# Performance work log

Hardware: AMD Instinct MI355X
Metric: run time of the kernel (lower is better)

The kernel has to match this reference:

```python
import jax, jax.numpy as jnp
import numpy as np

DIM = 1536
HEADS = 12
HD = DIM // HEADS  # 128
EPS = 1e-6
SINK_SIZE = 1          # frames
MAX_ATTN = 1920        # tokens (sliding window)


def setup_inputs() -> dict:
    key = jax.random.key(0)
    ks = jax.random.split(key, 10)
    B = 1
    F, H, W = 8, 16, 24
    L = F * H * W  # 3072
    s = 0.02
    inp = {
        "x": jax.random.normal(ks[0], (B, L, DIM), jnp.float32),
        "seq_lens": jnp.array([L], jnp.int32),
        "grid_sizes": jnp.array([[F, H, W]], jnp.int32),
        "freqs": jax.random.normal(ks[1], (1024, HD // 2, 2), jnp.float32),
        "wq": jax.random.normal(ks[2], (DIM, DIM), jnp.float32) * s,
        "bq": jnp.zeros((DIM,), jnp.float32),
        "wk": jax.random.normal(ks[3], (DIM, DIM), jnp.float32) * s,
        "bk": jnp.zeros((DIM,), jnp.float32),
        "wv": jax.random.normal(ks[4], (DIM, DIM), jnp.float32) * s,
        "bv": jnp.zeros((DIM,), jnp.float32),
        "wo": jax.random.normal(ks[5], (DIM, DIM), jnp.float32) * s,
        "bo": jnp.zeros((DIM,), jnp.float32),
        "nq_w": jnp.ones((DIM,), jnp.float32),
        "nk_w": jnp.ones((DIM,), jnp.float32),
    }
    return inp


def _rmsnorm(x, w):
    # WanRMSNorm: x * rsqrt(mean(x^2) + eps) * weight
    return x * jax.lax.rsqrt(jnp.mean(x * x, axis=-1, keepdims=True) + EPS) * w


def _rope(x, F, H, W, fc):
    # x: [B, L, n, d]; fc: complex [1024, d//2]
    B, L, n, d = x.shape
    c = d // 2
    c1 = c - 2 * (c // 3)  # temporal split
    c2 = c // 3
    f0, f1, f2 = fc[:, :c1], fc[:, c1:c1 + c2], fc[:, c1 + c2:]
    fr = jnp.concatenate([
        jnp.broadcast_to(f0[:F, None, None, :], (F, H, W, c1)),
        jnp.broadcast_to(f1[None, :H, None, :], (F, H, W, c2)),
        jnp.broadcast_to(f2[None, None, :W, :], (F, H, W, c2)),
    ], axis=-1).reshape(L, 1, c)  # [L, 1, c]
    xp = x.reshape(B, L, n, c, 2)
    xc = jax.lax.complex(xp[..., 0], xp[..., 1])  # [B, L, n, c]
    xr = xc * fr[None]
    return jnp.stack([jnp.real(xr), jnp.imag(xr)], axis=-1).reshape(B, L, n, d)


def reference(x, seq_lens, grid_sizes, freqs, wq, bq, wk, bk, wv, bv, wo, bo, nq_w, nk_w):
    B, L, _ = x.shape
    gs = np.asarray(grid_sizes)[0]
    F, H, W = int(gs[0]), int(gs[1]), int(gs[2])
    fs = H * W  # frame_seqlen
    sink = SINK_SIZE * fs

    q = _rmsnorm(x @ wq.T + bq, nq_w).reshape(B, L, HEADS, HD)
    k = _rmsnorm(x @ wk.T + bk, nk_w).reshape(B, L, HEADS, HD)
    v = (x @ wv.T + bv).reshape(B, L, HEADS, HD)

    fc = jax.lax.complex(freqs[..., 0], freqs[..., 1])  # [1024, HD//2]
    q = _rope(q, F, H, W, fc)
    k = _rope(k, F, H, W, fc)

    # sink + windowed frame-causal block mask (flex_attention block_mask)
    idx = jnp.arange(L)
    qf = idx // fs
    kf = idx // fs
    mask = (kf[None, :] <= qf[:, None]) & (
        (idx[None, :] < sink) | (idx[None, :] >= (qf[:, None] + 1) * fs - MAX_ATTN)
    )  # [L, L]

    scale = 1.0 / np.float32(np.sqrt(HD))
    scores = jnp.einsum('bqnd,bknd->bnqk', q, k) * scale
    scores = jnp.where(mask[None, None], scores, jnp.float32(-1e30))
    attn = jax.nn.softmax(scores, axis=-1)
    out = jnp.einsum('bnqk,bknd->bqnd', attn, v).reshape(B, L, DIM)
    return out @ wo.T + bo
```

## Files before the change

kernel.cpp:

```cpp
#include <hip/hip_runtime.h>
#include <stdint.h>

#define DIMC 1536
#define LTOK 3072
#define HEADS 12
#define HD 128
#define FS 384
#define MAXATTN 1920
#define HTOK 1152
#define NHT 1920

typedef __attribute__((ext_vector_type(4))) float f32x4;
typedef __attribute__((ext_vector_type(8))) short bf16x8;
typedef __attribute__((ext_vector_type(4))) unsigned int u32x4;

__device__ __forceinline__ unsigned short f2bf(float f) {
  union { float f; unsigned int u; } c; c.f = f;
  unsigned int u = c.u + 0x7fffu + ((c.u >> 16) & 1u);
  return (unsigned short)(u >> 16);
}
__device__ __forceinline__ float bf2f(unsigned short s) {
  union { unsigned int u; float f; } c; c.u = (unsigned int)s << 16; return c.f;
}

__device__ __forceinline__ void dma16(const void* g, void* l) {
  __builtin_amdgcn_global_load_lds(
      (const __attribute__((address_space(1))) unsigned int*)g,
      (__attribute__((address_space(3))) unsigned int*)l, 16, 0, 0);
}

__global__ __launch_bounds__(256)
void cvt_all_k(const float* __restrict__ x, const float* __restrict__ wq,
               const float* __restrict__ wk, const float* __restrict__ wv,
               const float* __restrict__ wo,
               unsigned short* __restrict__ xb, unsigned short* __restrict__ wqb,
               unsigned short* __restrict__ wkb, unsigned short* __restrict__ wvb,
               unsigned short* __restrict__ wob)
{
  const int i = blockIdx.x * 256 + threadIdx.x;
  const int n0 = LTOK * DIMC / 4;
  const int nw = DIMC * DIMC / 4;
  const float* src; unsigned short* dst; int off;
  if (i < n0) { src = x; dst = xb; off = i; }
  else {
    int j = i - n0; int w = j / nw; off = j - w * nw;
    src = (w == 0) ? wq : (w == 1) ? wk : (w == 2) ? wv : wo;
    dst = (w == 0) ? wqb : (w == 1) ? wkb : (w == 2) ? wvb : wob;
  }
  float4 f = ((const float4*)src)[off];
  uint2 o;
  o.x = (unsigned int)f2bf(f.x) | ((unsigned int)f2bf(f.y) << 16);
  o.y = (unsigned int)f2bf(f.z) | ((unsigned int)f2bf(f.w) << 16);
  ((uint2*)dst)[off] = o;
}

__global__ __launch_bounds__(256)
void gemm_qkv(const unsigned short* __restrict__ A,
              const unsigned short* __restrict__ B0,
              const unsigned short* __restrict__ B1,
              const unsigned short* __restrict__ B2,
              const float* __restrict__ bias0,
              const float* __restrict__ bias1,
              const float* __restrict__ bias2,
              unsigned short* __restrict__ o0, unsigned short* __restrict__ o1,
              unsigned short* __restrict__ o2)
{
  const int z = blockIdx.z;
  const unsigned short* Bw = (z == 0) ? B0 : (z == 1) ? B1 : B2;
  const float* bias = (z == 0) ? bias0 : (z == 1) ? bias1 : bias2;
  unsigned short* outp = (z == 0) ? o0 : (z == 1) ? o1 : o2;

  __shared__ __align__(16) unsigned short lA[128 * 32];
  __shared__ __align__(16) unsigned short lB[128 * 32];

  const int tid = threadIdx.x;
  const int wave = tid >> 6;
  const int lane = tid & 63;
  const int m0 = blockIdx.y * 128;
  const int n0 = blockIdx.x * 128;
  const int wm = (wave >> 1) * 64;
  const int wn = (wave & 1) * 64;

  f32x4 acc[4][4] = {};

  const int srow = tid >> 2;
  const int scol = (tid & 3) * 8;
  const int fr = lane & 15;
  const int fk = (lane >> 4) * 8;

  unsigned short* la0 = &lA[srow * 32 + scol];
  unsigned short* la1 = &lA[(srow + 64) * 32 + scol];
  unsigned short* lb0 = &lB[srow * 32 + scol];
  unsigned short* lb1 = &lB[(srow + 64) * 32 + scol];
  const unsigned short* ga0 = A  + (size_t)(m0 + srow)      * DIMC + scol;
  const unsigned short* ga1 = A  + (size_t)(m0 + srow + 64) * DIMC + scol;
  const unsigned short* gb0 = Bw + (size_t)(n0 + srow)      * DIMC + scol;
  const unsigned short* gb1 = Bw + (size_t)(n0 + srow + 64) * DIMC + scol;

  for (int k0 = 0; k0 < DIMC; k0 += 32) {
    dma16(ga0 + k0, la0);
    dma16(ga1 + k0, la1);
    dma16(gb0 + k0, lb0);
    dma16(gb1 + k0, lb1);
    __syncthreads();

    bf16x8 af[4], bf[4];
#pragma unroll
    for (int i = 0; i < 4; ++i)
      af[i] = *(const bf16x8*)&lA[(wm + i * 16 + fr) * 32 + fk];
#pragma unroll
    for (int j = 0; j < 4; ++j)
      bf[j] = *(const bf16x8*)&lB[(wn + j * 16 + fr) * 32 + fk];
#pragma unroll
    for (int i = 0; i < 4; ++i)
#pragma unroll
      for (int j = 0; j < 4; ++j)
        acc[i][j] = __builtin_amdgcn_mfma_f32_16x16x32_bf16(af[i], bf[j], acc[i][j], 0, 0, 0);
    __syncthreads();
  }

  const int col = lane & 15;
  const int rb = (lane >> 4) * 4;
#pragma unroll
  for (int j = 0; j < 4; ++j) {
    const int gn = n0 + wn + j * 16 + col;
    const float bv = bias[gn];
#pragma unroll
    for (int i = 0; i < 4; ++i)
#pragma unroll
      for (int r = 0; r < 4; ++r) {
        const int gm = m0 + wm + i * 16 + rb + r;
        outp[(size_t)gm * DIMC + gn] = f2bf(acc[i][j][r] + bv);
      }
  }
}

__global__ __launch_bounds__(512)
void gemm_wo(const unsigned short* __restrict__ A,
             const unsigned short* __restrict__ Bw,
             const float* __restrict__ bias,
             float* __restrict__ outp)
{
  __shared__ __align__(16) unsigned short lA[128 * 32];
  __shared__ __align__(16) unsigned short lB[128 * 32];

  const int tid = threadIdx.x;
  const int wave = tid >> 6;
  const int lane = tid & 63;
  const int m0 = blockIdx.y * 128;
  const int n0 = blockIdx.x * 128;
  const int wm = (wave >> 1) * 32;
  const int wn = (wave & 1) * 64;

  f32x4 acc[2][4] = {};

  const int srow = tid >> 2;
  const int scol = (tid & 3) * 8;
  const int fr = lane & 15;
  const int fk = (lane >> 4) * 8;

  unsigned short* la = &lA[srow * 32 + scol];
  unsigned short* lb = &lB[srow * 32 + scol];
  const unsigned short* ga = A  + (size_t)(m0 + srow) * DIMC + scol;
  const unsigned short* gb = Bw + (size_t)(n0 + srow) * DIMC + scol;

  for (int k0 = 0; k0 < DIMC; k0 += 32) {
    dma16(ga + k0, la);
    dma16(gb + k0, lb);
    __syncthreads();

    bf16x8 af[2], bf[4];
#pragma unroll
    for (int i = 0; i < 2; ++i)
      af[i] = *(const bf16x8*)&lA[(wm + i * 16 + fr) * 32 + fk];
#pragma unroll
    for (int j = 0; j < 4; ++j)
      bf[j] = *(const bf16x8*)&lB[(wn + j * 16 + fr) * 32 + fk];
#pragma unroll
    for (int i = 0; i < 2; ++i)
#pragma unroll
      for (int j = 0; j < 4; ++j)
        acc[i][j] = __builtin_amdgcn_mfma_f32_16x16x32_bf16(af[i], bf[j], acc[i][j], 0, 0, 0);
    __syncthreads();
  }

  const int col = lane & 15;
  const int rb = (lane >> 4) * 4;
#pragma unroll
  for (int j = 0; j < 4; ++j) {
    const int gn = n0 + wn + j * 16 + col;
    const float bv = bias[gn];
#pragma unroll
    for (int i = 0; i < 2; ++i)
#pragma unroll
      for (int r = 0; r < 4; ++r) {
        const int gm = m0 + wm + i * 16 + rb + r;
        outp[(size_t)gm * DIMC + gn] = acc[i][j][r] + bv;
      }
  }
}

__device__ __forceinline__ int vperm4(int G) {
  return (((G >> 3) & 1) << 3) | (((G >> 1) & 1) << 2) | ((G & 1) << 1) | ((G >> 2) & 1);
}

__global__ __launch_bounds__(256)
void post_qkv_k(unsigned short* __restrict__ q, unsigned short* __restrict__ k,
                const unsigned short* __restrict__ v, unsigned short* __restrict__ vt,
                const float* __restrict__ nqw, const float* __restrict__ nkw,
                const float* __restrict__ freqs)
{
  const int bx = blockIdx.x;
  const int tid = threadIdx.x;
  if (bx < 2 * LTOK) {
    const int which = bx >= LTOK;
    const int tok = bx - which * LTOK;
    unsigned short* row = (which ? k : q) + (size_t)tok * DIMC;
    const float* nw = which ? nkw : nqw;
    const float sc = which ? 1.f : (0.08838834764831845f * 1.4426950408889634f);
    const int base = tid * 6;

    float vv[6];
    float ss = 0.f;
#pragma unroll
    for (int j = 0; j < 6; ++j) {
      vv[j] = bf2f(row[base + j]);
      ss += vv[j] * vv[j];
    }
#pragma unroll
    for (int off = 1; off < 64; off <<= 1) ss += __shfl_xor(ss, off);
    __shared__ float wsum[4];
    if ((tid & 63) == 0) wsum[tid >> 6] = ss;
    __syncthreads();
    const float total = wsum[0] + wsum[1] + wsum[2] + wsum[3];
    const float rms = rsqrtf(total * (1.f / DIMC) + 1e-6f);

    const int f = tok / FS;
    const int rem = tok - f * FS;
    const int h = rem / 24;
    const int w = rem - h * 24;

#pragma unroll
    for (int pp = 0; pp < 3; ++pp) {
      const int P = (base >> 1) + pp;
      const int p = P & 63;
      const int t = (p < 22) ? f : ((p < 43) ? h : w);
      const float fre = freqs[t * 128 + p * 2];
      const float fim = freqs[t * 128 + p * 2 + 1];
      const float e = vv[2 * pp]     * rms * nw[base + 2 * pp];
      const float o = vv[2 * pp + 1] * rms * nw[base + 2 * pp + 1];
      row[base + 2 * pp]     = f2bf((e * fre - o * fim) * sc);
      row[base + 2 * pp + 1] = f2bf((e * fim + o * fre) * sc);
    }
  } else {
    const int c0 = bx - 2 * LTOK;
    const int tb = (c0 % 48) * 64;
    const int db = (c0 / 48) * 64;
    __shared__ __align__(16) unsigned short t[64 * 72];
#pragma unroll
    for (int it = 0; it < 2; ++it) {
      int c = tid + it * 256;
      int tok = c >> 3, dc = (c & 7) * 8;
      uint4 val = *(const uint4*)(v + (size_t)(tb + tok) * DIMC + db + dc);
      unsigned short tmp[8];
      *(uint4*)tmp = val;
#pragma unroll
      for (int j = 0; j < 8; ++j) t[(dc + j) * 72 + tok] = tmp[j];
    }
    __syncthreads();
#pragma unroll
    for (int it = 0; it < 4; ++it) {
      int c = tid + it * 256;
      int d = c >> 4, G = c & 15;
      *(uint2*)(vt + ((size_t)db + d) * LTOK + tb + vperm4(G) * 4) =
          *(const uint2*)&t[d * 72 + G * 4];
    }
  }
}

__global__ __launch_bounds__(256, 3)
void attn_flash(const unsigned short* __restrict__ q,
                const unsigned short* __restrict__ k,
                const unsigned short* __restrict__ vt,
                unsigned short* __restrict__ ab,
                float* __restrict__ Opart,
                float* __restrict__ mlbuf)
{
  const int bid = blockIdx.x;
  int qb, head, chunk, nchunks;
  if (bid < 360) { const int hb = bid >> 1; qb = 23 - hb / 12; head = hb % 12; chunk = bid & 1; nchunks = 2; }
  else           { const int lb = bid - 360; qb = 8 - lb / 12; head = lb % 12; chunk = 0; nchunks = 1; }

  const int q0 = qb * 128;
  const int qf = qb / 3;
  const int kend = (qf + 1) * FS;
  const int s2 = kend - MAXATTN;
  const bool two = (s2 > FS);
  const int nt1 = (two ? FS : kend) >> 6;
  const int nt  = nt1 + (two ? (MAXATTN >> 6) : 0);
  const int half = nt / nchunks;
  const int tstart = chunk * half, tend = tstart + half;

  const int tid = threadIdx.x;
  const int wave = tid >> 6, lane = tid & 63;
  const int col = lane & 15;
  const int g = lane >> 4;
  const int g4 = g * 4;

  __shared__ __align__(16) unsigned short Kl[64 * 128];
  __shared__ __align__(16) unsigned short Vtl[128 * 64];

  bf16x8 qfA[4], qfB[4];
  {
    const unsigned short* qr0 = q + (size_t)(q0 + wave * 32 + col) * DIMC + head * HD;
#pragma unroll
    for (int kk = 0; kk < 4; ++kk) {
      qfA[kk] = *(const bf16x8*)(qr0 + kk * 32 + g * 8);
      qfB[kk] = *(const bf16x8*)(qr0 + (size_t)16 * DIMC + kk * 32 + g * 8);
    }
  }

  f32x4 o0[8] = {}, o1[8] = {};
  float m0 = -3.0e38f, l0 = 0.f, m1 = -3.0e38f, l1 = 0.f;

  const int krow = tid >> 4;
  const int kc8  = ((tid & 15) ^ krow) * 8;
  const unsigned short* kg = k + (size_t)krow * DIMC + head * HD + kc8;
  const int vrow = tid >> 3;
  const int vc8  = ((tid & 7) ^ (vrow & 7)) * 8;
  const unsigned short* vg = vt + ((size_t)head * HD + vrow) * LTOK + vc8;
  unsigned short* kl = Kl + tid * 8;
  unsigned short* vl = Vtl + tid * 8;

  for (int t = tstart; t < tend; ++t) {
    const int kb = (t < nt1) ? t * 64 : s2 + (t - nt1) * 64;
    const unsigned short* kp = kg + (size_t)kb * DIMC;
    dma16(kp,                     kl);
    dma16(kp + (size_t)16 * DIMC, kl + 16 * 128);
    dma16(kp + (size_t)32 * DIMC, kl + 32 * 128);
    dma16(kp + (size_t)48 * DIMC, kl + 48 * 128);
    const unsigned short* vp = vg + kb;
    dma16(vp,                     vl);
    dma16(vp + (size_t)32 * LTOK, vl + 32 * 64);
    dma16(vp + (size_t)64 * LTOK, vl + 64 * 64);
    dma16(vp + (size_t)96 * LTOK, vl + 96 * 64);
    __syncthreads();

    f32x4 sA[4] = {}, sB[4] = {};
#pragma unroll
    for (int kt = 0; kt < 4; ++kt) {
      const unsigned short* kr = &Kl[(kt * 16 + col) * 128];
#pragma unroll
      for (int kk = 0; kk < 4; ++kk) {
        bf16x8 kfr = *(const bf16x8*)(kr + ((kk * 4 + g) ^ col) * 8);
        sA[kt] = __builtin_amdgcn_mfma_f32_16x16x32_bf16(kfr, qfA[kk], sA[kt], 0, 0, 0);
        sB[kt] = __builtin_amdgcn_mfma_f32_16x16x32_bf16(kfr, qfB[kk], sB[kt], 0, 0, 0);
      }
    }

    unsigned int A0, A1, A2, A3, A4, A5, A6, A7;
    float alA;
    {
      float mx = sA[0][0];
#pragma unroll
      for (int kt = 0; kt < 4; ++kt)
#pragma unroll
        for (int r = 0; r < 4; ++r) mx = fmaxf(mx, sA[kt][r]);
      mx = fmaxf(mx, __shfl_xor(mx, 16));
      mx = fmaxf(mx, __shfl_xor(mx, 32));
      const float mn = fmaxf(m0, mx);
      alA = exp2f(m0 - mn);
      m0 = mn;
      float rs = 0.f;
#define PKA(KT, PA, PB)                                        \
      {                                                        \
        const unsigned short p0 = f2bf(exp2f(sA[KT][0] - mn)); \
        const unsigned short p1 = f2bf(exp2f(sA[KT][1] - mn)); \
        const unsigned short p2 = f2bf(exp2f(sA[KT][2] - mn)); \
        const unsigned short p3 = f2bf(exp2f(sA[KT][3] - mn)); \
        rs += bf2f(p0) + bf2f(p1) + bf2f(p2) + bf2f(p3);       \
        PA = (unsigned int)p0 | ((unsigned int)p1 << 16);      \
        PB = (unsigned int)p2 | ((unsigned int)p3 << 16);      \
      }
      PKA(0, A0, A1) PKA(1, A2, A3) PKA(2, A4, A5) PKA(3, A6, A7)
#undef PKA
      rs += __shfl_xor(rs, 16);
      rs += __shfl_xor(rs, 32);
      l0 = l0 * alA + rs;
    }
    unsigned int B0, B1, B2, B3, B4, B5, B6, B7;
    float alB;
    {
      float mx = sB[0][0];
#pragma unroll
      for (int kt = 0; kt < 4; ++kt)
#pragma unroll
        for (int r = 0; r < 4; ++r) mx = fmaxf(mx, sB[kt][r]);
      mx = fmaxf(mx, __shfl_xor(mx, 16));
      mx = fmaxf(mx, __shfl_xor(mx, 32));
      const float mn = fmaxf(m1, mx);
      alB = exp2f(m1 - mn);
      m1 = mn;
      float rs = 0.f;
#define PKB(KT, PA, PB)                                        \
      {                                                        \
        const unsigned short p0 = f2bf(exp2f(sB[KT][0] - mn)); \
        const unsigned short p1 = f2bf(exp2f(sB[KT][1] - mn)); \
        const unsigned short p2 = f2bf(exp2f(sB[KT][2] - mn)); \
        const unsigned short p3 = f2bf(exp2f(sB[KT][3] - mn)); \
        rs += bf2f(p0) + bf2f(p1) + bf2f(p2) + bf2f(p3);       \
        PA = (unsigned int)p0 | ((unsigned int)p1 << 16);      \
        PB = (unsigned int)p2 | ((unsigned int)p3 << 16);      \
      }
      PKB(0, B0, B1) PKB(1, B2, B3) PKB(2, B4, B5) PKB(3, B6, B7)
#undef PKB
      rs += __shfl_xor(rs, 16);
      rs += __shfl_xor(rs, 32);
      l1 = l1 * alB + rs;
    }

#pragma unroll
    for (int dt = 0; dt < 8; ++dt) { o0[dt] *= alA; o1[dt] *= alB; }

    u32x4 tA0, tA1, tB0, tB1;
    tA0[0] = A0; tA0[1] = A1; tA0[2] = A2; tA0[3] = A3;
    tA1[0] = A4; tA1[1] = A5; tA1[2] = A6; tA1[3] = A7;
    tB0[0] = B0; tB0[1] = B1; tB0[2] = B2; tB0[3] = B3;
    tB1[0] = B4; tB1[1] = B5; tB1[2] = B6; tB1[3] = B7;
    const bf16x8 pfA0 = __builtin_bit_cast(bf16x8, tA0);
    const bf16x8 pfA1 = __builtin_bit_cast(bf16x8, tA1);
    const bf16x8 pfB0 = __builtin_bit_cast(bf16x8, tB0);
    const bf16x8 pfB1 = __builtin_bit_cast(bf16x8, tB1);

    const int vx0 = (g ^ (col & 7)) * 8;
    const int vx1 = ((4 + g) ^ (col & 7)) * 8;
#pragma unroll
    for (int dt = 0; dt < 8; ++dt) {
      const unsigned short* vr = &Vtl[(dt * 16 + col) * 64];
      bf16x8 vf0 = *(const bf16x8*)(vr + vx0);
      o0[dt] = __builtin_amdgcn_mfma_f32_16x16x32_bf16(vf0, pfA0, o0[dt], 0, 0, 0);
      o1[dt] = __builtin_amdgcn_mfma_f32_16x16x32_bf16(vf0, pfB0, o1[dt], 0, 0, 0);
      bf16x8 vf1 = *(const bf16x8*)(vr + vx1);
      o0[dt] = __builtin_amdgcn_mfma_f32_16x16x32_bf16(vf1, pfA1, o0[dt], 0, 0, 0);
      o1[dt] = __builtin_amdgcn_mfma_f32_16x16x32_bf16(vf1, pfB1, o1[dt], 0, 0, 0);
    }
    __syncthreads();
  }

  const int qrow0 = q0 + wave * 32 + col;
  if (nchunks == 1) {
    const float i0 = 1.f / l0, i1 = 1.f / l1;
    unsigned short* or0 = ab + (size_t)qrow0 * DIMC + head * HD;
    unsigned short* or1 = or0 + (size_t)16 * DIMC;
#pragma unroll
    for (int dt = 0; dt < 8; ++dt) {
      uint2 pk;
      pk.x = (unsigned int)f2bf(o0[dt][0] * i0) | ((unsigned int)f2bf(o0[dt][1] * i0) << 16);
      pk.y = (unsigned int)f2bf(o0[dt][2] * i0) | ((unsigned int)f2bf(o0[dt][3] * i0) << 16);
      *(uint2*)(or0 + dt * 16 + g4) = pk;
      pk.x = (unsigned int)f2bf(o1[dt][0] * i1) | ((unsigned int)f2bf(o1[dt][1] * i1) << 16);
      pk.y = (unsigned int)f2bf(o1[dt][2] * i1) | ((unsigned int)f2bf(o1[dt][3] * i1) << 16);
      *(uint2*)(or1 + dt * 16 + g4) = pk;
    }
  } else {
    const int tokp0 = qrow0 - HTOK;
    float* ob0 = Opart + ((size_t)(chunk * NHT + tokp0) * HEADS + head) * HD;
    float* ob1 = Opart + ((size_t)(chunk * NHT + tokp0 + 16) * HEADS + head) * HD;
#pragma unroll
    for (int dt = 0; dt < 8; ++dt) {
      *(f32x4*)(ob0 + dt * 16 + g4) = o0[dt];
      *(f32x4*)(ob1 + dt * 16 + g4) = o1[dt];
    }
    if (lane < 16) {
      float* mlp0 = mlbuf + 2 * ((size_t)(chunk * NHT + tokp0) * HEADS + head);
      float* mlp1 = mlbuf + 2 * ((size_t)(chunk * NHT + tokp0 + 16) * HEADS + head);
      mlp0[0] = m0; mlp0[1] = l0;
      mlp1[0] = m1; mlp1[1] = l1;
    }
  }
}

__global__ __launch_bounds__(384)
void merge_k(const float* __restrict__ Opart, const float* __restrict__ mlbuf,
             unsigned short* __restrict__ ab)
{
  const int tokp = blockIdx.x;
  const int tid = threadIdx.x;
  const int e = tid * 4;
  const int head = e >> 7;
  const size_t r0 = (size_t)tokp * DIMC + e;
  float4 o0 = *(const float4*)(Opart + r0);
  float4 o1 = *(const float4*)(Opart + (size_t)NHT * DIMC + r0);
  const float* ml0 = mlbuf + 2 * ((size_t)tokp * HEADS + head);
  const float* ml1 = mlbuf + 2 * ((size_t)(NHT + tokp) * HEADS + head);
  const float m0 = ml0[0], l0 = ml0[1], m1 = ml1[0], l1 = ml1[1];
  const float mm = fmaxf(m0, m1);
  const float a0 = exp2f(m0 - mm), a1 = exp2f(m1 - mm);
  const float inv = 1.f / (l0 * a0 + l1 * a1);
  uint2 pk;
  pk.x = (unsigned int)f2bf((o0.x * a0 + o1.x * a1) * inv) |
         ((unsigned int)f2bf((o0.y * a0 + o1.y * a1) * inv) << 16);
  pk.y = (unsigned int)f2bf((o0.z * a0 + o1.z * a1) * inv) |
         ((unsigned int)f2bf((o0.w * a0 + o1.w * a1) * inv) << 16);
  *(uint2*)(ab + (size_t)(HTOK + tokp) * DIMC + e) = pk;
}

extern "C" void kernel_launch(void* const* d_in, const int* in_sizes, int n_in,
                              void* d_out, int out_size, void* d_ws, size_t ws_size,
                              hipStream_t stream)
{
  (void)in_sizes; (void)n_in; (void)out_size; (void)ws_size;
  const float* x     = (const float*)d_in[0];
  const float* freqs = (const float*)d_in[3];
  const float* wq    = (const float*)d_in[4];
  const float* bq    = (const float*)d_in[5];
  const float* wk    = (const float*)d_in[6];
  const float* bk    = (const float*)d_in[7];
  const float* wv    = (const float*)d_in[8];
  const float* bv    = (const float*)d_in[9];
  const float* wo    = (const float*)d_in[10];
  const float* bo    = (const float*)d_in[11];
  const float* nqw   = (const float*)d_in[12];
  const float* nkw   = (const float*)d_in[13];

  char* ws = (char*)d_ws;
  size_t off = 0;
  auto take = [&](size_t bytes) -> void* {
    void* p = ws + off; off += (bytes + 255) & ~(size_t)255; return p;
  };
  unsigned short* wob = (unsigned short*)take((size_t)DIMC * DIMC * 2);
  unsigned short* qb  = (unsigned short*)take((size_t)LTOK * DIMC * 2);
  unsigned short* kb  = (unsigned short*)take((size_t)LTOK * DIMC * 2);
  unsigned short* vb  = (unsigned short*)take((size_t)LTOK * DIMC * 2);
  unsigned short* ab  = (unsigned short*)take((size_t)LTOK * DIMC * 2);
  unsigned short* vtb = (unsigned short*)take((size_t)LTOK * DIMC * 2);
  unsigned short* xb  = (unsigned short*)take((size_t)LTOK * DIMC * 2);
  unsigned short* wqb = (unsigned short*)take((size_t)DIMC * DIMC * 2);
  unsigned short* wkb = (unsigned short*)take((size_t)DIMC * DIMC * 2);
  unsigned short* wvb = (unsigned short*)take((size_t)DIMC * DIMC * 2);
  float* mlb = (float*)take((size_t)2 * NHT * HEADS * 2 * sizeof(float));
  float* Opart = (float*)xb;

  cvt_all_k<<<dim3(13824), dim3(256), 0, stream>>>(x, wq, wk, wv, wo,
                                                   xb, wqb, wkb, wvb, wob);

  gemm_qkv<<<dim3(DIMC / 128, LTOK / 128, 3), dim3(256), 0, stream>>>(
      xb, wqb, wkb, wvb, bq, bk, bv, qb, kb, vb);

  post_qkv_k<<<dim3(2 * LTOK + 1152), dim3(256), 0, stream>>>(
      qb, kb, vb, vtb, nqw, nkw, freqs);

  attn_flash<<<dim3(468), dim3(256), 0, stream>>>(qb, kb, vtb, ab, Opart, mlb);
  merge_k<<<dim3(NHT), dim3(384), 0, stream>>>(Opart, mlb, ab);

  gemm_wo<<<dim3(DIMC / 128, LTOK / 128), dim3(512), 0, stream>>>(
      ab, wob, bo, (float*)d_out);
}
```

Baseline: 319.4 us.

## Double-buffer LDS tiles in GEMMs and flash attention to overlap loads

After: 318.5 us. Within noise of the previous version (-0.3%).

```diff
diff --git a/kernel.cpp b/kernel.cpp
--- a/kernel.cpp
+++ b/kernel.cpp
@@ -54,6 +54,7 @@
   ((uint2*)dst)[off] = o;
 }
 
+#define GBUF (128 * 32)
 __global__ __launch_bounds__(256)
 void gemm_qkv(const unsigned short* __restrict__ A,
               const unsigned short* __restrict__ B0,
@@ -70,8 +71,8 @@
   const float* bias = (z == 0) ? bias0 : (z == 1) ? bias1 : bias2;
   unsigned short* outp = (z == 0) ? o0 : (z == 1) ? o1 : o2;
 
-  __shared__ __align__(16) unsigned short lA[128 * 32];
-  __shared__ __align__(16) unsigned short lB[128 * 32];
+  __shared__ __align__(16) unsigned short lA[2 * GBUF];
+  __shared__ __align__(16) unsigned short lB[2 * GBUF];
 
   const int tid = threadIdx.x;
   const int wave = tid >> 6;
@@ -88,35 +89,42 @@
   const int fr = lane & 15;
   const int fk = (lane >> 4) * 8;
 
-  unsigned short* la0 = &lA[srow * 32 + scol];
-  unsigned short* la1 = &lA[(srow + 64) * 32 + scol];
-  unsigned short* lb0 = &lB[srow * 32 + scol];
-  unsigned short* lb1 = &lB[(srow + 64) * 32 + scol];
+  unsigned short* laS = lA + srow * 32 + scol;
+  unsigned short* lbS = lB + srow * 32 + scol;
   const unsigned short* ga0 = A  + (size_t)(m0 + srow)      * DIMC + scol;
   const unsigned short* ga1 = A  + (size_t)(m0 + srow + 64) * DIMC + scol;
   const unsigned short* gb0 = Bw + (size_t)(n0 + srow)      * DIMC + scol;
   const unsigned short* gb1 = Bw + (size_t)(n0 + srow + 64) * DIMC + scol;
 
-  for (int k0 = 0; k0 < DIMC; k0 += 32) {
-    dma16(ga0 + k0, la0);
-    dma16(ga1 + k0, la1);
-    dma16(gb0 + k0, lb0);
-    dma16(gb1 + k0, lb1);
+  dma16(ga0, laS);
+  dma16(ga1, laS + 64 * 32);
+  dma16(gb0, lbS);
+  dma16(gb1, lbS + 64 * 32);
+
+  for (int t = 0; t < 48; ++t) {
+    const int cur = (t & 1) * GBUF;
     __syncthreads();
+    if (t < 47) {
+      const int nxt = GBUF - cur;
+      const int k0n = (t + 1) * 32;
+      dma16(ga0 + k0n, laS + nxt);
+      dma16(ga1 + k0n, laS + nxt + 64 * 32);
+      dma16(gb0 + k0n, lbS + nxt);
+      dma16(gb1 + k0n, lbS + nxt + 64 * 32);
+    }
 
     bf16x8 af[4], bf[4];
 #pragma unroll
     for (int i = 0; i < 4; ++i)
-      af[i] = *(const bf16x8*)&lA[(wm + i * 16 + fr) * 32 + fk];
+      af[i] = *(const bf16x8*)&lA[cur + (wm + i * 16 + fr) * 32 + fk];
 #pragma unroll
     for (int j = 0; j < 4; ++j)
-      bf[j] = *(const bf16x8*)&lB[(wn + j * 16 + fr) * 32 + fk];
+      bf[j] = *(const bf16x8*)&lB[cur + (wn + j * 16 + fr) * 32 + fk];
 #pragma unroll
     for (int i = 0; i < 4; ++i)
 #pragma unroll
       for (int j = 0; j < 4; ++j)
         acc[i][j] = __builtin_amdgcn_mfma_f32_16x16x32_bf16(af[i], bf[j], acc[i][j], 0, 0, 0);
-    __syncthreads();
   }
 
   const int col = lane & 15;
@@ -141,8 +149,8 @@
              const float* __restrict__ bias,
              float* __restrict__ outp)
 {
-  __shared__ __align__(16) unsigned short lA[128 * 32];
-  __shared__ __align__(16) unsigned short lB[128 * 32];
+  __shared__ __align__(16) unsigned short lA[2 * GBUF];
+  __shared__ __align__(16) unsigned short lB[2 * GBUF];
 
   const int tid = threadIdx.x;
   const int wave = tid >> 6;
@@ -159,29 +167,36 @@
   const int fr = lane & 15;
   const int fk = (lane >> 4) * 8;
 
-  unsigned short* la = &lA[srow * 32 + scol];
-  unsigned short* lb = &lB[srow * 32 + scol];
+  unsigned short* laS = lA + srow * 32 + scol;
+  unsigned short* lbS = lB + srow * 32 + scol;
   const unsigned short* ga = A  + (size_t)(m0 + srow) * DIMC + scol;
   const unsigned short* gb = Bw + (size_t)(n0 + srow) * DIMC + scol;
 
-  for (int k0 = 0; k0 < DIMC; k0 += 32) {
-    dma16(ga + k0, la);
-    dma16(gb + k0, lb);
+  dma16(ga, laS);
+  dma16(gb, lbS);
+
+  for (int t = 0; t < 48; ++t) {
+    const int cur = (t & 1) * GBUF;
     __syncthreads();
+    if (t < 47) {
+      const int nxt = GBUF - cur;
+      const int k0n = (t + 1) * 32;
+      dma16(ga + k0n, laS + nxt);
+      dma16(gb + k0n, lbS + nxt);
+    }
 
     bf16x8 af[2], bf[4];
 #pragma unroll
     for (int i = 0; i < 2; ++i)
-      af[i] = *(const bf16x8*)&lA[(wm + i * 16 + fr) * 32 + fk];
+      af[i] = *(const bf16x8*)&lA[cur + (wm + i * 16 + fr) * 32 + fk];
 #pragma unroll
     for (int j = 0; j < 4; ++j)
-      bf[j] = *(const bf16x8*)&lB[(wn + j * 16 + fr) * 32 + fk];
+      bf[j] = *(const bf16x8*)&lB[cur + (wn + j * 16 + fr) * 32 + fk];
 #pragma unroll
     for (int i = 0; i < 2; ++i)
 #pragma unroll
       for (int j = 0; j < 4; ++j)
         acc[i][j] = __builtin_amdgcn_mfma_f32_16x16x32_bf16(af[i], bf[j], acc[i][j], 0, 0, 0);
-    __syncthreads();
   }
 
   const int col = lane & 15;
@@ -278,7 +293,9 @@
   }
 }
 
-__global__ __launch_bounds__(256, 3)
+#define KBUF (64 * 128)
+#define VBUF (128 * 64)
+__global__ __launch_bounds__(256, 2)
 void attn_flash(const unsigned short* __restrict__ q,
                 const unsigned short* __restrict__ k,
                 const unsigned short* __restrict__ vt,
@@ -307,8 +324,8 @@
   const int g = lane >> 4;
   const int g4 = g * 4;
 
-  __shared__ __align__(16) unsigned short Kl[64 * 128];
-  __shared__ __align__(16) unsigned short Vtl[128 * 64];
+  __shared__ __align__(16) unsigned short Kl[2 * KBUF];
+  __shared__ __align__(16) unsigned short Vtl[2 * VBUF];
 
   bf16x8 qfA[4], qfB[4];
   {
@@ -332,8 +349,8 @@
   unsigned short* kl = Kl + tid * 8;
   unsigned short* vl = Vtl + tid * 8;
 
-  for (int t = tstart; t < tend; ++t) {
-    const int kb = (t < nt1) ? t * 64 : s2 + (t - nt1) * 64;
+  {
+    const int kb = (tstart < nt1) ? tstart * 64 : s2 + (tstart - nt1) * 64;
     const unsigned short* kp = kg + (size_t)kb * DIMC;
     dma16(kp,                     kl);
     dma16(kp + (size_t)16 * DIMC, kl + 16 * 128);
@@ -344,12 +361,32 @@
     dma16(vp + (size_t)32 * LTOK, vl + 32 * 64);
     dma16(vp + (size_t)64 * LTOK, vl + 64 * 64);
     dma16(vp + (size_t)96 * LTOK, vl + 96 * 64);
+  }
+
+  for (int t = tstart; t < tend; ++t) {
+    const int kcur = ((t - tstart) & 1) * KBUF;
+    const int vcur = ((t - tstart) & 1) * VBUF;
     __syncthreads();
 
+    if (t + 1 < tend) {
+      const int kb = (t + 1 < nt1) ? (t + 1) * 64 : s2 + (t + 1 - nt1) * 64;
+      const int knxt = KBUF - kcur, vnxt = VBUF - vcur;
+      const unsigned short* kp = kg + (size_t)kb * DIMC;
+      dma16(kp,                     kl + knxt);
+      dma16(kp + (size_t)16 * DIMC, kl + knxt + 16 * 128);
+      dma16(kp + (size_t)32 * DIMC, kl + knxt + 32 * 128);
+      dma16(kp + (size_t)48 * DIMC, kl + knxt + 48 * 128);
+      const unsigned short* vp = vg + kb;
+      dma16(vp,                     vl + vnxt);
+      dma16(vp + (size_t)32 * LTOK, vl + vnxt + 32 * 64);
+      dma16(vp + (size_t)64 * LTOK, vl + vnxt + 64 * 64);
+      dma16(vp + (size_t)96 * LTOK, vl + vnxt + 96 * 64);
+    }
+
     f32x4 sA[4] = {}, sB[4] = {};
 #pragma unroll
     for (int kt = 0; kt < 4; ++kt) {
-      const unsigned short* kr = &Kl[(kt * 16 + col) * 128];
+      const unsigned short* kr = &Kl[kcur + (kt * 16 + col) * 128];
 #pragma unroll
       for (int kk = 0; kk < 4; ++kk) {
         bf16x8 kfr = *(const bf16x8*)(kr + ((kk * 4 + g) ^ col) * 8);
@@ -436,7 +473,7 @@
     const int vx1 = ((4 + g) ^ (col & 7)) * 8;
 #pragma unroll
     for (int dt = 0; dt < 8; ++dt) {
-      const unsigned short* vr = &Vtl[(dt * 16 + col) * 64];
+      const unsigned short* vr = &Vtl[vcur + (dt * 16 + col) * 64];
       bf16x8 vf0 = *(const bf16x8*)(vr + vx0);
       o0[dt] = __builtin_amdgcn_mfma_f32_16x16x32_bf16(vf0, pfA0, o0[dt], 0, 0, 0);
       o1[dt] = __builtin_amdgcn_mfma_f32_16x16x32_bf16(vf0, pfB0, o1[dt], 0, 0, 0);
@@ -444,7 +481,6 @@
       o0[dt] = __builtin_amdgcn_mfma_f32_16x16x32_bf16(vf1, pfA1, o0[dt], 0, 0, 0);
       o1[dt] = __builtin_amdgcn_mfma_f32_16x16x32_bf16(vf1, pfB1, o1[dt], 0, 0, 0);
     }
-    __syncthreads();
   }
 
   const int qrow0 = q0 + wave * 32 + col;
```
